# Kernel optimization log

Measured on AMD Instinct MI355X. Metric: run time of the kernel, lower is better.

## Reference

```python
import jax, jax.numpy as jnp
import numpy as np

B, S, HID = 2, 2048, 2048
NK, NV, DK, DV, K = 16, 32, 128, 128, 4
KEY_DIM = NK * DK          # 2048
VAL_DIM = NV * DV          # 4096
CONV_DIM = 2 * KEY_DIM + VAL_DIM  # 8192
EPS = 1e-6


def setup_inputs() -> dict:
    key = jax.random.key(0)
    ks = jax.random.split(key, 8)
    n = lambda k, shape, sc: jax.random.normal(k, shape, jnp.float32) * sc
    return {
        "hidden_states": n(ks[0], (B, S, HID), 1.0),
        "W_qkv": n(ks[1], (CONV_DIM, HID), 0.02),
        "W_z": n(ks[2], (VAL_DIM, HID), 0.02),
        "W_b": n(ks[3], (NV, HID), 0.02),
        "W_a": n(ks[4], (NV, HID), 0.02),
        "conv_w": n(ks[5], (CONV_DIM, K), 0.3),   # depthwise conv weight, squeeze(1) of [C,1,K]
        "norm_w": jnp.ones((DV,), jnp.float32),
        "W_out": n(ks[6], (HID, VAL_DIM), 0.02),
        "dt_bias": jnp.ones((NV,), jnp.float32),
        "A_log": jnp.zeros((NV,), jnp.float32),
    }


def _l2norm(t):
    return t * jax.lax.rsqrt(jnp.sum(t * t, axis=-1, keepdims=True) + EPS)


def _forward(hidden_states, W_qkv, W_z, W_b, W_a, conv_w, norm_w, W_out, dt_bias, A_log):
    b_, s_, _ = hidden_states.shape
    mixed = hidden_states @ W_qkv.T                     # [B,S,CONV_DIM]
    z = (hidden_states @ W_z.T).reshape(b_, s_, NV, DV)  # gate branch
    b_proj = hidden_states @ W_b.T                      # [B,S,NV]
    a_proj = hidden_states @ W_a.T                      # [B,S,NV]

    # causal depthwise conv1d (groups=CONV_DIM, no bias) + silu
    x = jnp.transpose(mixed, (0, 2, 1))                 # [B,C,S]
    x = jnp.pad(x, ((0, 0), (0, 0), (K - 1, 0)))
    x = jax.lax.conv_general_dilated(
        x, conv_w[:, None, :], window_strides=(1,), padding="VALID",
        feature_group_count=CONV_DIM)
    mixed = jnp.transpose(jax.nn.silu(x), (0, 2, 1))    # [B,S,CONV_DIM]

    q, k, v = jnp.split(mixed, [KEY_DIM, 2 * KEY_DIM], axis=-1)
    q = q.reshape(b_, s_, NK, DK)
    k = k.reshape(b_, s_, NK, DK)
    v = v.reshape(b_, s_, NV, DV)

    beta = jax.nn.sigmoid(b_proj)                                    # [B,S,NV]
    g = -jnp.exp(A_log) * jax.nn.softplus(a_proj + dt_bias)          # [B,S,NV], log decay

    rep = NV // NK
    q = jnp.repeat(q, rep, axis=2)                      # GQA expand -> [B,S,NV,DK]
    k = jnp.repeat(k, rep, axis=2)
    q = _l2norm(q)
    k = _l2norm(k)
    scale = DK ** -0.5

    def step(state, inp):  # state: [B,NV,DK,DV]
        qt, kt, vt, gt, bt = inp  # [B,NV,DK],[B,NV,DK],[B,NV,DV],[B,NV],[B,NV]
        state = state * jnp.exp(gt)[..., None, None]
        mem = jnp.einsum('bhk,bhkv->bhv', kt, state)
        delta = (vt - mem) * bt[..., None]
        state = state + jnp.einsum('bhk,bhv->bhkv', kt, delta)
        ot = jnp.einsum('bhk,bhkv->bhv', qt * scale, state)
        return state, ot

    init = jnp.zeros((b_, NV, DK, DV), jnp.float32)
    xs = (jnp.moveaxis(q, 1, 0), jnp.moveaxis(k, 1, 0), jnp.moveaxis(v, 1, 0),
          jnp.moveaxis(g, 1, 0), jnp.moveaxis(beta, 1, 0))
    _, o = jax.lax.scan(step, init, xs)                 # [S,B,NV,DV]
    o = jnp.moveaxis(o, 0, 1)                           # [B,S,NV,DV]

    # RMSNormGated over head_v_dim, then silu(z) gate
    var = jnp.mean(o * o, axis=-1, keepdims=True)
    o = o * jax.lax.rsqrt(var + EPS) * norm_w
    o = (o * jax.nn.silu(z)).reshape(b_, s_, VAL_DIM)
    return o @ W_out.T


def reference(hidden_states, W_qkv, W_z, W_b, W_a, conv_w, norm_w, W_out, dt_bias, A_log):
    return _forward(hidden_states, W_qkv, W_z, W_b, W_a, conv_w, norm_w, W_out, dt_bias, A_log)
```

## Files before the change

### kernel.cpp

```cpp
#include <hip/hip_runtime.h>
#include <hip/hip_bf16.h>
#include <math.h>

#define DEVI __device__ __forceinline__

typedef __attribute__((ext_vector_type(4))) float f32x4;
typedef __attribute__((ext_vector_type(8))) short s16x8;
typedef __attribute__((ext_vector_type(4))) unsigned int u32x4;

DEVI float bf2f(ushort u){ union{unsigned int i; float f;} x; x.i = ((unsigned int)u)<<16; return x.f; }
DEVI ushort f2bf(float f){ union{float f; unsigned int i;} x; x.f = f;
  unsigned int r = x.i + 0x7fffu + ((x.i>>16)&1u); return (ushort)(r>>16); }

#define MFMA16(a,b,c) __builtin_amdgcn_mfma_f32_16x16x32_bf16(a,b,c,0,0,0)

__global__ __launch_bounds__(256) void cvt_bf16(const float* __restrict__ in, ushort* __restrict__ out){
  int i = blockIdx.x*256 + threadIdx.x;
  float4 v = ((const float4*)in)[i];
  ushort4 o; o.x = f2bf(v.x); o.y = f2bf(v.y); o.z = f2bf(v.z); o.w = f2bf(v.w);
  ((ushort4*)out)[i] = o;
}

DEVI void gl_lds16(const ushort* g, ushort* l){
  __builtin_amdgcn_global_load_lds((const __attribute__((address_space(1))) void*)g,
                                   (__attribute__((address_space(3))) void*)l, 16, 0, 0);
}

#define SBAR() __builtin_amdgcn_s_barrier()
#define LGKM0() do{ asm volatile("s_waitcnt lgkmcnt(0)" ::: "memory"); __builtin_amdgcn_sched_barrier(0); }while(0)
#define VMC6() asm volatile("s_waitcnt vmcnt(6)" ::: "memory")
#define VMC4() asm volatile("s_waitcnt vmcnt(4)" ::: "memory")

template<int BF16_OUT>
__global__ __launch_bounds__(512, 2) void gemm256(const ushort* __restrict__ A,
                                                  const ushort* __restrict__ B,
                                                  void* __restrict__ Cv,
                                                  int M, int N, int K,
                                                  int rpx, int cpx){
  __shared__ ushort smem[65536];
  __shared__ ushort dummy[4096];
  const int tid = threadIdx.x, w = tid>>6, lane = tid&63;
  const int fr = lane&15, quad = lane>>4;
  const int wm = w>>2, wn = w&3;
  const int NT = K>>6;

  const int nbn = N>>8;
  const int bid = blockIdx.x;
  const int xcd = bid & 7, idx = bid >> 3;
  const int CGn = nbn / cpx;
  const int rgrp = xcd / CGn, cgrp = xcd % CGn;
  const int rloc = idx % rpx, cloc = idx / rpx;
  const long tileM = (long)(rgrp*rpx + rloc) << 8;
  const long tileN = (long)(cgrp*cpx + cloc) << 8;

  const int rr  = (tid&63)>>2;
  const int cc  = ((tid&3)*8) ^ ((rr&8)?16:0);
  const int row0 = (w>>1)*16 + rr;
  const int col0 = (w&1)*32 + cc;
  const long off0 = (long)row0*K + col0;
  const long h64 = 64l*K;

  const ushort* pA0 = A + tileM*K + off0;
  const ushort* pA1 = pA0 + 128l*K;
  const ushort* pB0 = B + tileN*K + off0;
  const ushort* pB1 = pB0 + 128l*K;

  const int dw = w*512;
  ushort* dmy = dummy + dw;

#define ST_A0(bb,tt) do{ if((tt)<NT){ const long kk=(long)(tt)<<6; \
    gl_lds16(pA0+kk, smem+(bb)*32768+dw);        gl_lds16(pA1+kk, smem+(bb)*32768+8192+dw);} \
    else { gl_lds16(pA0, dmy); gl_lds16(pA1, dmy);} }while(0)
#define ST_A1(bb,tt) do{ if((tt)<NT){ const long kk=((long)(tt)<<6)+h64; \
    gl_lds16(pA0+kk, smem+(bb)*32768+4096+dw);   gl_lds16(pA1+kk, smem+(bb)*32768+12288+dw);} \
    else { gl_lds16(pA0, dmy); gl_lds16(pA1, dmy);} }while(0)
#define ST_B0(bb,tt) do{ if((tt)<NT){ const long kk=(long)(tt)<<6; \
    gl_lds16(pB0+kk, smem+(bb)*32768+16384+dw);  gl_lds16(pB1+kk, smem+(bb)*32768+24576+dw);} \
    else { gl_lds16(pB0, dmy); gl_lds16(pB1, dmy);} }while(0)
#define ST_B1(bb,tt) do{ if((tt)<NT){ const long kk=((long)(tt)<<6)+h64; \
    gl_lds16(pB0+kk, smem+(bb)*32768+20480+dw);  gl_lds16(pB1+kk, smem+(bb)*32768+28672+dw);} \
    else { gl_lds16(pB0, dmy); gl_lds16(pB1, dmy);} }while(0)

  const int baseF = fr*32 + ((quad*8) ^ ((fr&8)?16:0));
  const int sB = (wn&1)*4;

  f32x4 acc[8][4];
  #pragma unroll
  for (int i=0;i<8;i++)
    #pragma unroll
    for (int j=0;j<4;j++) acc[i][j] = (f32x4){0.f,0.f,0.f,0.f};

  ST_A0(0,0); ST_B0(0,0); ST_B1(0,0); ST_A1(0,0);
  ST_A0(1,1); ST_B0(1,1); ST_B1(1,1);
  VMC6();
  SBAR();

  #pragma unroll 2
  for (int t=0; t<NT; ++t){
    const int bs = t&1;
    const ushort* SA = smem + bs*32768 + wm*8192;
    const ushort* SB = smem + bs*32768 + 16384 + (wn>>1)*8192;
    s16x8 af[4][2], bl[2][2], bh[2][2];
    #pragma unroll
    for (int mt=0;mt<4;mt++)
      #pragma unroll
      for (int ks=0;ks<2;ks++)
        af[mt][ks] = *(const s16x8*)(SA + ((mt*2+ks)<<9) + baseF);
    #pragma unroll
    for (int nt=0;nt<2;nt++)
      #pragma unroll
      for (int ks=0;ks<2;ks++)
        bl[nt][ks] = *(const s16x8*)(SB + (((sB+nt)*2+ks)<<9) + baseF);
    ST_A1(bs^1, t+1);
    SBAR(); LGKM0();
    __builtin_amdgcn_s_setprio(1);
    #pragma unroll
    for (int mt=0;mt<4;mt++)
      #pragma unroll
      for (int nt=0;nt<2;nt++){
        acc[mt][nt] = MFMA16(af[mt][0], bl[nt][0], acc[mt][nt]);
        acc[mt][nt] = MFMA16(af[mt][1], bl[nt][1], acc[mt][nt]);
      }
    __builtin_amdgcn_s_setprio(0);
    SBAR();
    #pragma unroll
    for (int nt=0;nt<2;nt++)
      #pragma unroll
      for (int ks=0;ks<2;ks++)
        bh[nt][ks] = *(const s16x8*)(SB + (((sB+2+nt)*2+ks)<<9) + baseF);
    ST_A0(bs, t+2);
    SBAR(); LGKM0();
    __builtin_amdgcn_s_setprio(1);
    #pragma unroll
    for (int mt=0;mt<4;mt++)
      #pragma unroll
      for (int nt=0;nt<2;nt++){
        acc[mt][2+nt] = MFMA16(af[mt][0], bh[nt][0], acc[mt][2+nt]);
        acc[mt][2+nt] = MFMA16(af[mt][1], bh[nt][1], acc[mt][2+nt]);
      }
    __builtin_amdgcn_s_setprio(0);
    SBAR();
    #pragma unroll
    for (int mt=0;mt<4;mt++)
      #pragma unroll
      for (int ks=0;ks<2;ks++)
        af[mt][ks] = *(const s16x8*)(SA + (((4+mt)*2+ks)<<9) + baseF);
    ST_B0(bs, t+2);
    SBAR(); LGKM0();
    __builtin_amdgcn_s_setprio(1);
    #pragma unroll
    for (int mt=0;mt<4;mt++)
      #pragma unroll
      for (int nt=0;nt<2;nt++){
        acc[4+mt][nt] = MFMA16(af[mt][0], bl[nt][0], acc[4+mt][nt]);
        acc[4+mt][nt] = MFMA16(af[mt][1], bl[nt][1], acc[4+mt][nt]);
      }
    __builtin_amdgcn_s_setprio(0);
    SBAR();
    ST_B1(bs, t+2);
    SBAR();
    __builtin_amdgcn_s_setprio(1);
    #pragma unroll
    for (int mt=0;mt<4;mt++)
      #pragma unroll
      for (int nt=0;nt<2;nt++){
        acc[4+mt][2+nt] = MFMA16(af[mt][0], bh[nt][0], acc[4+mt][2+nt]);
        acc[4+mt][2+nt] = MFMA16(af[mt][1], bh[nt][1], acc[4+mt][2+nt]);
      }
    __builtin_amdgcn_s_setprio(0);
    VMC6();
    SBAR();
  }
#undef ST_A0
#undef ST_A1
#undef ST_B0
#undef ST_B1

  const long Rb = tileM + wm*128 + quad*4;
  const long Cb = tileN + wn*64 + fr;
  if (BF16_OUT){
    ushort* C = (ushort*)Cv;
    #pragma unroll
    for (int mt=0;mt<8;mt++)
      #pragma unroll
      for (int r=0;r<4;r++){
        const long row = Rb + mt*16 + r;
        #pragma unroll
        for (int nt=0;nt<4;nt++)
          C[row*(long)N + Cb + nt*16] = f2bf(acc[mt][nt][r]);
      }
  } else {
    float* C = (float*)Cv;
    #pragma unroll
    for (int mt=0;mt<8;mt++)
      #pragma unroll
      for (int r=0;r<4;r++){
        const long row = Rb + mt*16 + r;
        #pragma unroll
        for (int nt=0;nt<4;nt++)
          C[row*(long)N + Cb + nt*16] = acc[mt][nt][r];
      }
  }
}

template<int BF16_OUT>
__global__ __launch_bounds__(512, 2) void gemm256n128(const ushort* __restrict__ A,
                                                      const ushort* __restrict__ B,
                                                      void* __restrict__ Cv,
                                                      int M, int N, int K,
                                                      int rpx, int cpx){
  __shared__ ushort smem[49152];
  __shared__ ushort dummy[4096];
  const int tid = threadIdx.x, w = tid>>6, lane = tid&63;
  const int fr = lane&15, quad = lane>>4;
  const int wm = w>>2, wn = w&3;
  const int NT = K>>6;

  const int nbn = N>>7;
  const int bid = blockIdx.x;
  const int xcd = bid & 7, idx = bid >> 3;
  const int CGn = nbn / cpx;
  const int rgrp = xcd / CGn, cgrp = xcd % CGn;
  const int rloc = idx % rpx, cloc = idx / rpx;
  const long tileM = (long)(rgrp*rpx + rloc) << 8;
  const long tileN = (long)(cgrp*cpx + cloc) << 7;

  const int rr  = (tid&63)>>2;
  const int cc  = ((tid&3)*8) ^ ((rr&8)?16:0);
  const int row0 = (w>>1)*16 + rr;
  const int col0 = (w&1)*32 + cc;
  const long off0 = (long)row0*K + col0;
  const long h64 = 64l*K;

  const ushort* pA0 = A + tileM*K + off0;
  const ushort* pA1 = pA0 + 128l*K;
  const ushort* pB0 = B + tileN*K + off0;

  const int dw = w*512;
  ushort* dmy = dummy + dw;

#define ST_A0(bb,tt) do{ if((tt)<NT){ const long kk=(long)(tt)<<6; \
    gl_lds16(pA0+kk, smem+(bb)*24576+dw);        gl_lds16(pA1+kk, smem+(bb)*24576+8192+dw);} \
    else { gl_lds16(pA0, dmy); gl_lds16(pA1, dmy);} }while(0)
#define ST_A1(bb,tt) do{ if((tt)<NT){ const long kk=((long)(tt)<<6)+h64; \
    gl_lds16(pA0+kk, smem+(bb)*24576+4096+dw);   gl_lds16(pA1+kk, smem+(bb)*24576+12288+dw);} \
    else { gl_lds16(pA0, dmy); gl_lds16(pA1, dmy);} }while(0)
#define ST_B(bb,tt) do{ if((tt)<NT){ const long kk=(long)(tt)<<6; \
    gl_lds16(pB0+kk, smem+(bb)*24576+16384+dw);  gl_lds16(pB0+kk+h64, smem+(bb)*24576+20480+dw);} \
    else { gl_lds16(pB0, dmy); gl_lds16(pB0, dmy);} }while(0)

  const int baseF = fr*32 + ((quad*8) ^ ((fr&8)?16:0));

  f32x4 acc[8][2];
  #pragma unroll
  for (int i=0;i<8;i++)
    #pragma unroll
    for (int j=0;j<2;j++) acc[i][j] = (f32x4){0.f,0.f,0.f,0.f};

  ST_A0(0,0); ST_B(0,0); ST_A1(0,0);
  ST_A0(1,1); ST_B(1,1);
  VMC4();
  SBAR();

  #pragma unroll 2
  for (int t=0; t<NT; ++t){
    const int bs = t&1;
    const ushort* SA = smem + bs*24576 + wm*8192;
    const ushort* SB = smem + bs*24576 + 16384;
    s16x8 af[4][2], bl[2], bh[2];
    #pragma unroll
    for (int mt=0;mt<4;mt++)
      #pragma unroll
      for (int ks=0;ks<2;ks++)
        af[mt][ks] = *(const s16x8*)(SA + ((mt*2+ks)<<9) + baseF);
    #pragma unroll
    for (int ks=0;ks<2;ks++)
      bl[ks] = *(const s16x8*)(SB + (((wn*2+0)*2+ks)<<9) + baseF);
    ST_A1(bs^1, t+1);
    SBAR(); LGKM0();
    __builtin_amdgcn_s_setprio(1);
    #pragma unroll
    for (int mt=0;mt<4;mt++){
      acc[mt][0] = MFMA16(af[mt][0], bl[0], acc[mt][0]);
      acc[mt][0] = MFMA16(af[mt][1], bl[1], acc[mt][0]);
    }
    __builtin_amdgcn_s_setprio(0);
    SBAR();
    #pragma unroll
    for (int ks=0;ks<2;ks++)
      bh[ks] = *(const s16x8*)(SB + (((wn*2+1)*2+ks)<<9) + baseF);
    ST_A0(bs, t+2);
    SBAR(); LGKM0();
    __builtin_amdgcn_s_setprio(1);
    #pragma unroll
    for (int mt=0;mt<4;mt++){
      acc[mt][1] = MFMA16(af[mt][0], bh[0], acc[mt][1]);
      acc[mt][1] = MFMA16(af[mt][1], bh[1], acc[mt][1]);
    }
    __builtin_amdgcn_s_setprio(0);
    SBAR();
    #pragma unroll
    for (int mt=0;mt<4;mt++)
      #pragma unroll
      for (int ks=0;ks<2;ks++)
        af[mt][ks] = *(const s16x8*)(SA + (((4+mt)*2+ks)<<9) + baseF);
    ST_B(bs, t+2);
    SBAR(); LGKM0();
    __builtin_amdgcn_s_setprio(1);
    #pragma unroll
    for (int mt=0;mt<4;mt++){
      acc[4+mt][0] = MFMA16(af[mt][0], bl[0], acc[4+mt][0]);
      acc[4+mt][0] = MFMA16(af[mt][1], bl[1], acc[4+mt][0]);
    }
    __builtin_amdgcn_s_setprio(0);
    SBAR();
    __builtin_amdgcn_s_setprio(1);
    #pragma unroll
    for (int mt=0;mt<4;mt++){
      acc[4+mt][1] = MFMA16(af[mt][0], bh[0], acc[4+mt][1]);
      acc[4+mt][1] = MFMA16(af[mt][1], bh[1], acc[4+mt][1]);
    }
    __builtin_amdgcn_s_setprio(0);
    VMC4();
    SBAR();
  }
#undef ST_A0
#undef ST_A1
#undef ST_B

  const long Rb = tileM + wm*128 + quad*4;
  const long Cb = tileN + wn*32 + fr;
  if (BF16_OUT){
    ushort* C = (ushort*)Cv;
    #pragma unroll
    for (int mt=0;mt<8;mt++)
      #pragma unroll
      for (int r=0;r<4;r++){
        const long row = Rb + mt*16 + r;
        #pragma unroll
        for (int nt=0;nt<2;nt++)
          C[row*(long)N + Cb + nt*16] = f2bf(acc[mt][nt][r]);
      }
  } else {
    float* C = (float*)Cv;
    #pragma unroll
    for (int mt=0;mt<8;mt++)
      #pragma unroll
      for (int r=0;r<4;r++){
        const long row = Rb + mt*16 + r;
        #pragma unroll
        for (int nt=0;nt<2;nt++)
          C[row*(long)N + Cb + nt*16] = acc[mt][nt][r];
      }
  }
}

template<int BF16_OUT>
__global__ __launch_bounds__(256, 2) void gemm_bt(const ushort* __restrict__ A,
                                                  const ushort* __restrict__ B,
                                                  void* __restrict__ Cv,
                                                  int M, int N, int K){
  __shared__ ushort As[128*32];
  __shared__ ushort Bs[128*32];
  const int nb = N >> 7;
  const int tile_m = (blockIdx.x / nb) << 7;
  const int tile_n = (blockIdx.x % nb) << 7;
  const int tid  = threadIdx.x;
  const int w    = tid >> 6;
  const int lane = tid & 63;

  const int ca = w*2;
  const long rowA = tile_m + ca*16 + (lane>>2);
  const long rowB = tile_n + ca*16 + (lane>>2);
  const int  colE = (lane&3)*8;
  const ushort* pA0 = A + rowA*(long)K + colE;
  const ushort* pA1 = pA0 + 16l*K;
  const ushort* pB0 = B + rowB*(long)K + colE;
  const ushort* pB1 = pB0 + 16l*K;
  ushort* lA0 = As + ca*512;
  ushort* lA1 = As + ca*512 + 512;
  ushort* lB0 = Bs + ca*512;
  ushort* lB1 = Bs + ca*512 + 512;

  const int wr = (w>>1)<<6;
  const int wc = (w&1)<<6;
  const int fr = lane & 15;
  const int fk = (lane>>4)<<3;

  f32x4 acc[4][4];
  #pragma unroll
  for (int i=0;i<4;i++)
    #pragma unroll
    for (int j=0;j<4;j++) acc[i][j] = (f32x4){0.f,0.f,0.f,0.f};

  for (int k0 = 0; k0 < K; k0 += 32){
    __syncthreads();
    gl_lds16(pA0, lA0);
    gl_lds16(pA1, lA1);
    gl_lds16(pB0, lB0);
    gl_lds16(pB1, lB1);
    __syncthreads();
    s16x8 af[4], bfr[4];
    #pragma unroll
    for (int t=0;t<4;t++){
      af[t]  = *(const s16x8*)(As + (wr + t*16 + fr)*32 + fk);
      bfr[t] = *(const s16x8*)(Bs + (wc + t*16 + fr)*32 + fk);
    }
    #pragma unroll
    for (int mt=0;mt<4;mt++)
      #pragma unroll
      for (int nt=0;nt<4;nt++)
        acc[mt][nt] = MFMA16(af[mt], bfr[nt], acc[mt][nt]);
    pA0 += 32; pA1 += 32; pB0 += 32; pB1 += 32;
  }

  const int crow = tile_m + wr + ((lane>>4)<<2);
  const int ccol = tile_n + wc + (lane&15);
  if (BF16_OUT){
    ushort* C = (ushort*)Cv;
    #pragma unroll
    for (int mt=0;mt<4;mt++)
      #pragma unroll
      for (int r=0;r<4;r++){
        long row = crow + mt*16 + r;
        #pragma unroll
        for (int nt=0;nt<4;nt++)
          C[row*(long)N + ccol + nt*16] = f2bf(acc[mt][nt][r]);
      }
  } else {
    float* C = (float*)Cv;
    #pragma unroll
    for (int mt=0;mt<4;mt++)
      #pragma unroll
      for (int r=0;r<4;r++){
        long row = crow + mt*16 + r;
        #pragma unroll
        for (int nt=0;nt<4;nt++)
          C[row*(long)N + ccol + nt*16] = acc[mt][nt][r];
      }
  }
}

__global__ __launch_bounds__(256) void ba_post(const float* __restrict__ bapr,
    const float* __restrict__ dtb, const float* __restrict__ alog,
    float* __restrict__ beta, float* __restrict__ glog){
  const int idx = blockIdx.x*256 + threadIdx.x;
  const int m = idx >> 6, j = idx & 63;
  const float v = bapr[(long)m*128 + j];
  if (j < 32){
    beta[(long)m*32 + j] = 1.f/(1.f+expf(-v));
  } else {
    const int n = j - 32;
    float ap = v + dtb[n];
    float sp = (ap > 20.f) ? ap : log1pf(expf(ap));
    glog[(long)m*32 + n] = -expf(alog[n]) * sp;
  }
}

__global__ __launch_bounds__(256) void conv_qkv2(const ushort* __restrict__ mixed,
    const float* __restrict__ convw, ushort* __restrict__ qn, ushort* __restrict__ kn,
    ushort* __restrict__ vv){
  const long m0 = (long)blockIdx.x * 32;
  const int ct = blockIdx.y;
  const int ch = (ct<<11) + threadIdx.x*8;
  const ushort* base = mixed + ch;

  ushort* outp; int mode; float qsc = 1.f;
  if (ct == 0){ outp = qn + ch;        mode = 0; qsc = 0.08838834764831845f; }
  else if (ct == 1){ outp = kn + (ch-2048); mode = 1; }
  else { outp = vv + (ch-4096); mode = 2; }

  float cw0[8], cw1[8], cw2[8], cw3[8];
  #pragma unroll
  for (int e=0;e<8;e++){
    float4 wv = *(const float4*)(convw + (long)(ch+e)*4);
    cw0[e]=wv.x; cw1[e]=wv.y; cw2[e]=wv.z; cw3[e]=wv.w;
  }

#define LDROW(PTR, R) do{ s16x8 _v = *(const s16x8*)(PTR); \
    _Pragma("unroll") \
    for (int e=0;e<8;e++) R[e] = bf2f((ushort)_v[e]); }while(0)

#define STEP(P0,P1,P2,P3,MR) do{ \
    float y[8]; float ss = 0.f; \
    _Pragma("unroll") \
    for (int e=0;e<8;e++){ \
      float a = P0[e]*cw0[e]; \
      a += P1[e]*cw1[e]; \
      a += P2[e]*cw2[e]; \
      a += P3[e]*cw3[e]; \
      float sv = a / (1.f + expf(-a)); \
      y[e] = sv; ss += sv*sv; } \
    if (mode < 2){ \
      ss += __shfl_xor(ss,1); ss += __shfl_xor(ss,2); \
      ss += __shfl_xor(ss,4); ss += __shfl_xor(ss,8); \
      const float r_ = rsqrtf(ss + 1e-6f) * qsc; \
      s16x8 ov; \
      _Pragma("unroll") \
      for (int e=0;e<8;e++) ov[e] = (short)f2bf(y[e]*r_); \
      *(s16x8*)(outp + (MR)*2048) = ov; \
    } else { \
      s16x8 ov; \
      _Pragma("unroll") \
      for (int e=0;e<8;e++) ov[e] = (short)f2bf(y[e]); \
      *(s16x8*)(outp + (MR)*4096) = ov; \
    } \
  }while(0)

  float w3[8], w2[8], w1[8];
  if (((int)m0 & 2047) == 0){
    #pragma unroll
    for (int e=0;e<8;e++){ w3[e]=0.f; w2[e]=0.f; w1[e]=0.f; }
  } else {
    LDROW(base + (m0-3)*8192, w3);
    LDROW(base + (m0-2)*8192, w2);
    LDROW(base + (m0-1)*8192, w1);
  }

  long m = m0;
  for (int it=0; it<8; ++it){
    float r0[8], r1[8], r2[8], r3[8];
    LDROW(base + (m+0)*8192, r0);
    LDROW(base + (m+1)*8192, r1);
    LDROW(base + (m+2)*8192, r2);
    LDROW(base + (m+3)*8192, r3);
    STEP(w3,w2,w1,r0, m+0);
    STEP(w2,w1,r0,r1, m+1);
    STEP(w1,r0,r1,r2, m+2);
    STEP(r0,r1,r2,r3, m+3);
    #pragma unroll
    for (int e=0;e<8;e++){ w3[e]=r1[e]; w2[e]=r2[e]; w1[e]=r3[e]; }
    m += 4;
  }
#undef LDROW
#undef STEP
}

__global__ __launch_bounds__(256) void chunk_prep(
    const ushort* __restrict__ qn, const ushort* __restrict__ kn,
    const float* __restrict__ beta, const float* __restrict__ glog,
    ushort* __restrict__ Tg, ushort* __restrict__ Mg, float* __restrict__ cumLgG){
  const int bid = blockIdx.x;
  const int bh = bid >> 6, ch = bid & 63;
  const int b = bh>>5, h = bh&31, hq = h>>1;
  const long tch = (long)b*2048 + ch*32;
  const int tid = threadIdx.x, w = tid>>6, lane = tid&63;
  const int quad = lane>>4, l15 = lane&15;

  __shared__ __attribute__((aligned(16))) ushort Kl[32][136];
  __shared__ __attribute__((aligned(16))) ushort Ql[32][136];
  __shared__ float Asl[32][33];
  __shared__ float Lgl[32], Btl[32];

  const int sc = tid>>3, ss = (tid&7)*16;
  {
    const ushort* kp = kn + (tch+sc)*2048 + hq*128 + ss;
    const ushort* qp = qn + (tch+sc)*2048 + hq*128 + ss;
    *(u32x4*)&Kl[sc][ss] = *(const u32x4*)kp; *(u32x4*)&Kl[sc][ss+8] = *(const u32x4*)(kp+8);
    *(u32x4*)&Ql[sc][ss] = *(const u32x4*)qp; *(u32x4*)&Ql[sc][ss+8] = *(const u32x4*)(qp+8);
  }
  if (tid < 64){
    const int c = lane & 31;
    float gv = glog[(tch + c)*32 + h];
    float bv = beta[(tch + c)*32 + h];
    #pragma unroll
    for (int off=1; off<32; off<<=1){
      float t = __shfl_up(gv, off);
      if ((lane & 31) >= off) gv += t;
    }
    if (lane < 32){ Lgl[c] = gv; Btl[c] = bv; cumLgG[(long)bid*32 + c] = gv; }
  }
  __syncthreads();

  const int mt = w>>1, nt = w&1;
  s16x8 ka[4], qa[4], kb[4];
  #pragma unroll
  for (int ks=0; ks<4; ks++){
    ka[ks] = *(const s16x8*)&Kl[mt*16+l15][ks*32 + quad*8];
    qa[ks] = *(const s16x8*)&Ql[mt*16+l15][ks*32 + quad*8];
    kb[ks] = *(const s16x8*)&Kl[nt*16+l15][ks*32 + quad*8];
  }
  f32x4 accK = (f32x4){0.f,0.f,0.f,0.f}, accQ = (f32x4){0.f,0.f,0.f,0.f};
  #pragma unroll
  for (int ks=0; ks<4; ks++){
    accK = MFMA16(ka[ks], kb[ks], accK);
    accQ = MFMA16(qa[ks], kb[ks], accQ);
  }
  const int j = nt*16 + l15;
  const float Lgj = Lgl[j];
  #pragma unroll
  for (int i=0;i<4;i++){
    const int r = mt*16 + quad*4 + i;
    const float e = expf(Lgl[r]-Lgj);
    Asl[r][j] = (r>j) ? -Btl[r]*e*accK[i] : 0.f;
    Mg[(long)bid*1024 + r*32 + j] = (r>=j) ? f2bf(e*accQ[i]) : (ushort)0;
  }
  __syncthreads();

  if (tid < 32){
    const int jc = tid;
    float tc[32];
    #pragma unroll
    for (int c=0;c<32;c++){
      float acc = (c==jc) ? 1.f : 0.f;
      #pragma unroll
      for (int i2=0;i2<c;i2++) acc = fmaf(Asl[c][i2], tc[i2], acc);
      tc[c] = acc;
      Tg[(long)bid*1024 + c*32 + jc] = f2bf(acc);
    }
  }
}

__global__ __launch_bounds__(256, 2) void chunk_scan3(
    const ushort* __restrict__ qn, const ushort* __restrict__ kn,
    const ushort* __restrict__ vv, const float* __restrict__ beta,
    const float* __restrict__ cumLg, const ushort* __restrict__ Tg,
    const ushort* __restrict__ Mg, float* __restrict__ o){
  const int bh = blockIdx.x & 63, sl = blockIdx.x >> 6;
  const int b = bh>>5, h = bh&31, hq = h>>1;
  const int dv0 = sl<<4;
  const int tid = threadIdx.x, w = tid>>6, lane = tid&63;
  const int quad = lane>>4, l15 = lane&15;
  const int rt = w&1, kq = w>>1;

  __shared__ __attribute__((aligned(16))) ushort STl[16][136];
  __shared__ __attribute__((aligned(16))) ushort B0T[16][40];
  __shared__ __attribute__((aligned(16))) ushort DT[16][40];
  __shared__ float Btf[32], eLgl[32], eDf[32];

  const ushort* pKQ = (kq ? qn : kn) + ((long)b*2048 + rt*16 + l15)*2048 + hq*128 + quad*8;
  const ushort* pKT = kn + ((long)b*2048 + quad*8)*2048 + hq*128 + w*32 + l15;
  const ushort* pV  = vv + ((long)b*2048 + rt*16 + quad*4)*4096 + h*128 + dv0 + l15;
  const ushort* pTM = (kq ? Mg : Tg) + (long)bh*65536 + (rt*16 + l15)*32 + quad*8;
  const long pbBase = (long)bh*2048 + tid;
  const float* betaP = beta + ((long)b*2048 + tid)*32 + h;

  s16x8 cKQ[4], nKQ[4], cK0, cK1, nK0, nK1, cTM, nTM;
  ushort cV0=0,cV1=0,cV2=0,cV3=0, nV0=0,nV1=0,nV2=0,nV3=0;
  float cLg = 0.f, nLg = 0.f, cBt = 0.f, nBt = 0.f;

  f32x4 S0 = (f32x4){0.f,0.f,0.f,0.f}, S1 = (f32x4){0.f,0.f,0.f,0.f};

#define LOADCH(PKQ,PK0,PK1,PV0,PV1,PV2,PV3,PTMv,PLG,PBT,CH) do{ \
    const long co = (long)(CH)*65536; \
    _Pragma("unroll") \
    for (int ks=0; ks<4; ks++) PKQ[ks] = *(const s16x8*)(pKQ + co + ks*32); \
    _Pragma("unroll") \
    for (int e=0; e<8; e++){ \
      PK0[e] = (short)pKT[co + (long)e*2048]; \
      PK1[e] = (short)pKT[co + (long)e*2048 + 16]; } \
    if (kq == 0){ \
      const long vo = (long)(CH)*131072; \
      PV0 = pV[vo]; PV1 = pV[vo+4096]; PV2 = pV[vo+8192]; PV3 = pV[vo+12288]; } \
    PTMv = *(const s16x8*)(pTM + (long)(CH)*1024); \
    if (tid < 32){ PLG = cumLg[pbBase + (long)(CH)*32]; PBT = betaP[(long)(CH)*1024]; } \
  }while(0)

  LOADCH(cKQ, cK0, cK1, cV0,cV1,cV2,cV3, cTM, cLg, cBt, 0);

  for (int ch=0; ch<64; ch++){
    const long tch = (long)b*2048 + ch*32;
    LOADCH(nKQ, nK0, nK1, nV0,nV1,nV2,nV3, nTM, nLg, nBt, (ch<63)?(ch+1):63);
    if (tid < 32){
      float lgC = __shfl(cLg, 31);
      Btf[tid] = cBt;
      eLgl[tid] = expf(cLg);
      eDf[tid]  = expf(lgC - cLg);
    }
    {
      ushort4 p0, p1;
      p0.x=f2bf(S0[0]); p0.y=f2bf(S0[1]); p0.z=f2bf(S0[2]); p0.w=f2bf(S0[3]);
      p1.x=f2bf(S1[0]); p1.y=f2bf(S1[1]); p1.z=f2bf(S1[2]); p1.w=f2bf(S1[3]);
      *(ushort4*)&STl[l15][w*32 + quad*4]      = p0;
      *(ushort4*)&STl[l15][w*32 + 16 + quad*4] = p1;
    }
    __syncthreads();
    f32x4 acc = (f32x4){0.f,0.f,0.f,0.f};
    #pragma unroll
    for (int ks=0; ks<4; ks++){
      s16x8 sb = *(const s16x8*)&STl[l15][ks*32 + quad*8];
      acc = MFMA16(cKQ[ks], sb, acc);
    }
    if (kq == 0){
      const int c0r = rt*16 + quad*4;
      ushort4 pb;
      pb.x = f2bf(Btf[c0r+0]*(bf2f(cV0) - eLgl[c0r+0]*acc[0]));
      pb.y = f2bf(Btf[c0r+1]*(bf2f(cV1) - eLgl[c0r+1]*acc[1]));
      pb.z = f2bf(Btf[c0r+2]*(bf2f(cV2) - eLgl[c0r+2]*acc[2]));
      pb.w = f2bf(Btf[c0r+3]*(bf2f(cV3) - eLgl[c0r+3]*acc[3]));
      *(ushort4*)&B0T[l15][rt*16 + quad*4] = pb;
    } else {
      #pragma unroll
      for (int i=0;i<4;i++) acc[i] *= eLgl[rt*16 + quad*4 + i];
    }
    __syncthreads();
    const float eC = eLgl[31];
    s16x8 kta0, kta1;
    #pragma unroll
    for (int e=0;e<8;e++){
      const float ed = eDf[quad*8 + e];
      kta0[e] = (short)f2bf(bf2f((ushort)cK0[e])*ed);
      kta1[e] = (short)f2bf(bf2f((ushort)cK1[e])*ed);
    }
    if (kq == 0){
      s16x8 a = *(const s16x8*)&B0T[l15][quad*8];
      f32x4 Dt = MFMA16(a, cTM, ((f32x4){0.f,0.f,0.f,0.f}));
      #pragma unroll
      for (int i=0;i<4;i++)
        DT[quad*4+i][rt*16 + l15] = f2bf(Dt[i]);
    }
    __syncthreads();
    s16x8 df = *(const s16x8*)&DT[l15][quad*8];
    if (kq == 1){
      f32x4 O = MFMA16(cTM, df, acc);
      #pragma unroll
      for (int i=0;i<4;i++)
        o[(tch + rt*16 + quad*4 + i)*4096 + h*128 + dv0 + l15] = O[i];
    }
    f32x4 t0, t1;
    #pragma unroll
    for (int i=0;i<4;i++){ t0[i] = S0[i]*eC; t1[i] = S1[i]*eC; }
    S0 = MFMA16(kta0, df, t0);
    S1 = MFMA16(kta1, df, t1);
    #pragma unroll
    for (int ks=0; ks<4; ks++) cKQ[ks] = nKQ[ks];
    cK0 = nK0; cK1 = nK1; cTM = nTM;
    cV0 = nV0; cV1 = nV1; cV2 = nV2; cV3 = nV3;
    cLg = nLg; cBt = nBt;
  }
#undef LOADCH
}

__global__ __launch_bounds__(128) void norm_gate(const float* __restrict__ o,
    const ushort* __restrict__ z, const float* __restrict__ normw,
    ushort* __restrict__ og){
  const long mh = blockIdx.x;
  const int d = threadIdx.x;
  float x = o[mh*128 + d];
  float ss = x*x;
  #pragma unroll
  for (int off=32; off; off>>=1) ss += __shfl_xor(ss, off);
  __shared__ float w2[2];
  if ((d&63)==0) w2[d>>6] = ss;
  __syncthreads();
  float r = rsqrtf((w2[0]+w2[1])*(1.f/128.f) + 1e-6f);
  float zz = bf2f(z[mh*128 + d]);
  float sil = zz / (1.f + expf(-zz));
  og[mh*128 + d] = f2bf(x*r*normw[d]*sil);
}

extern "C" void kernel_launch(void* const* d_in, const int* in_sizes, int n_in,
                              void* d_out, int out_size, void* d_ws, size_t ws_size,
                              hipStream_t stream){
  const float* hs    = (const float*)d_in[0];
  const float* Wqkv  = (const float*)d_in[1];
  const float* Wz    = (const float*)d_in[2];
  const float* Wb    = (const float*)d_in[3];
  const float* Wa    = (const float*)d_in[4];
  const float* convw = (const float*)d_in[5];
  const float* normw = (const float*)d_in[6];
  const float* Wout  = (const float*)d_in[7];
  const float* dtb   = (const float*)d_in[8];
  const float* alog  = (const float*)d_in[9];

  char* ws = (char*)d_ws;
  ushort* hsb   = (ushort*)(ws);
  ushort* wqb   = (ushort*)(ws + (16l<<20));
  ushort* wzb   = (ushort*)(ws + (48l<<20));
  ushort* wob   = (ushort*)(ws + (64l<<20));
  ushort* mixed = (ushort*)(ws + (80l<<20));
  ushort* zb    = (ushort*)(ws + (144l<<20));
  float*  beta  = (float*)(ws + (176l<<20));
  float*  cumLg = (float*)(ws + (176l<<20) + (512l<<10));
  float*  glog  = (float*)(ws + (177l<<20));
  ushort* Tg    = (ushort*)(ws + (178l<<20));
  ushort* Mg    = (ushort*)(ws + (186l<<20));
  ushort* wbab  = (ushort*)(ws + (194l<<20));
  float*  bapr  = (float*)(ws + (195l<<20));
  ushort* kn = hsb;  ushort* qn = wzb;  ushort* vvp = wqb;  ushort* og = wqb;
  float*  o_raw = (float*)mixed;

  cvt_bf16<<<8192,  256, 0, stream>>>(hs,   hsb);
  cvt_bf16<<<16384, 256, 0, stream>>>(Wqkv, wqb);
  cvt_bf16<<<8192,  256, 0, stream>>>(Wz,   wzb);
  cvt_bf16<<<8192,  256, 0, stream>>>(Wout, wob);
  cvt_bf16<<<64,    256, 0, stream>>>(Wb,   wbab);
  cvt_bf16<<<64,    256, 0, stream>>>(Wa,   wbab + 65536);

  gemm256<1><<<512, 512, 0, stream>>>(hsb, wqb, (void*)mixed, 4096, 8192, 2048, 4, 16);
  gemm256<1><<<256, 512, 0, stream>>>(hsb, wzb, (void*)zb,    4096, 4096, 2048, 4, 8);
  gemm_bt<0><<<32*1,  256, 0, stream>>>(hsb, wbab, (void*)bapr, 4096, 128,  2048);
  ba_post<<<1024, 256, 0, stream>>>(bapr, dtb, alog, beta, glog);

  conv_qkv2<<<dim3(128,4), 256, 0, stream>>>(mixed, convw, qn, kn, vvp);
  chunk_prep<<<4096, 256, 0, stream>>>(qn, kn, beta, glog, Tg, Mg, cumLg);
  chunk_scan3<<<512, 256, 0, stream>>>(qn, kn, vvp, beta, cumLg, Tg, Mg, o_raw);
  norm_gate<<<131072, 128, 0, stream>>>(o_raw, zb, normw, og);

  gemm256n128<0><<<256, 512, 0, stream>>>(og, wob, d_out, 4096, 2048, 4096, 4, 8);
}
```

Before: 697.8 us.

## Restructure GEMM mainloop to triple-buffered BK=32 stages with simpler schedule

Replaces the double-buffered BK=64 GEMM mainloop, which interleaved partial LDS loads with four MFMA sub-phases, with a triple-buffered BK=32 pipeline. Each iteration issues one stage load two steps ahead, waits on vmcnt, reads all A/B fragments and runs all 32 MFMAs. LDS use shrinks and the LDS swizzle changes to a new XOR pattern. The aim is deeper prefetch with fewer barriers per MFMA, at the cost of half the K work per barrier pair and less overlap of LDS reads with MFMA.

```diff
diff --git a/kernel.cpp b/kernel.cpp
--- a/kernel.cpp
+++ b/kernel.cpp
@@ -28,7 +28,7 @@
 
 #define SBAR() __builtin_amdgcn_s_barrier()
 #define LGKM0() do{ asm volatile("s_waitcnt lgkmcnt(0)" ::: "memory"); __builtin_amdgcn_sched_barrier(0); }while(0)
-#define VMC6() asm volatile("s_waitcnt vmcnt(6)" ::: "memory")
+#define VMC8() asm volatile("s_waitcnt vmcnt(8)" ::: "memory")
 #define VMC4() asm volatile("s_waitcnt vmcnt(4)" ::: "memory")
 
 template<int BF16_OUT>
@@ -37,12 +37,12 @@
                                                   void* __restrict__ Cv,
                                                   int M, int N, int K,
                                                   int rpx, int cpx){
-  __shared__ ushort smem[65536];
+  __shared__ ushort smem[49152];
   __shared__ ushort dummy[4096];
   const int tid = threadIdx.x, w = tid>>6, lane = tid&63;
   const int fr = lane&15, quad = lane>>4;
   const int wm = w>>2, wn = w&3;
-  const int NT = K>>6;
+  const int NT2 = K>>5;
 
   const int nbn = N>>8;
   const int bid = blockIdx.x;
@@ -53,36 +53,24 @@
   const long tileM = (long)(rgrp*rpx + rloc) << 8;
   const long tileN = (long)(cgrp*cpx + cloc) << 8;
 
-  const int rr  = (tid&63)>>2;
-  const int cc  = ((tid&3)*8) ^ ((rr&8)?16:0);
-  const int row0 = (w>>1)*16 + rr;
-  const int col0 = (w&1)*32 + cc;
-  const long off0 = (long)row0*K + col0;
-  const long h64 = 64l*K;
-
-  const ushort* pA0 = A + tileM*K + off0;
-  const ushort* pA1 = pA0 + 128l*K;
-  const ushort* pB0 = B + tileN*K + off0;
-  const ushort* pB1 = pB0 + 128l*K;
-
-  const int dw = w*512;
-  ushort* dmy = dummy + dw;
-
-#define ST_A0(bb,tt) do{ if((tt)<NT){ const long kk=(long)(tt)<<6; \
-    gl_lds16(pA0+kk, smem+(bb)*32768+dw);        gl_lds16(pA1+kk, smem+(bb)*32768+8192+dw);} \
-    else { gl_lds16(pA0, dmy); gl_lds16(pA1, dmy);} }while(0)
-#define ST_A1(bb,tt) do{ if((tt)<NT){ const long kk=((long)(tt)<<6)+h64; \
-    gl_lds16(pA0+kk, smem+(bb)*32768+4096+dw);   gl_lds16(pA1+kk, smem+(bb)*32768+12288+dw);} \
-    else { gl_lds16(pA0, dmy); gl_lds16(pA1, dmy);} }while(0)
-#define ST_B0(bb,tt) do{ if((tt)<NT){ const long kk=(long)(tt)<<6; \
-    gl_lds16(pB0+kk, smem+(bb)*32768+16384+dw);  gl_lds16(pB1+kk, smem+(bb)*32768+24576+dw);} \
-    else { gl_lds16(pB0, dmy); gl_lds16(pB1, dmy);} }while(0)
-#define ST_B1(bb,tt) do{ if((tt)<NT){ const long kk=((long)(tt)<<6)+h64; \
-    gl_lds16(pB0+kk, smem+(bb)*32768+20480+dw);  gl_lds16(pB1+kk, smem+(bb)*32768+28672+dw);} \
-    else { gl_lds16(pB0, dmy); gl_lds16(pB1, dmy);} }while(0)
-
-  const int baseF = fr*32 + ((quad*8) ^ ((fr&8)?16:0));
-  const int sB = (wn&1)*4;
+  const int srow = lane>>2;
+  const int scol = ((lane&3) ^ ((lane>>3)&3))*8;
+  const ushort* pSA = A + (tileM + w*16 + srow)*(long)K + scol;
+  const ushort* pSB = B + (tileN + w*16 + srow)*(long)K + scol;
+  const long h128 = 128l*K;
+  const int dwv = w*512;
+  ushort* dmy = dummy + dwv;
+
+#define STG(bb,tt) do{ if((tt)<NT2){ const long kk=(long)(tt)<<5; \
+    gl_lds16(pSA+kk,      smem+(bb)*16384+dwv); \
+    gl_lds16(pSA+kk+h128, smem+(bb)*16384+4096+dwv); \
+    gl_lds16(pSB+kk,      smem+(bb)*16384+8192+dwv); \
+    gl_lds16(pSB+kk+h128, smem+(bb)*16384+12288+dwv); } \
+    else { gl_lds16(pSA,dmy); gl_lds16(pSA,dmy); gl_lds16(pSB,dmy); gl_lds16(pSB,dmy);} }while(0)
+
+  const int swz = (quad ^ ((fr>>1)&3))*8;
+  const int laneA = (wm*128 + fr)*32 + swz;
+  const int laneB = 8192 + (wn*64 + fr)*32 + swz;
 
   f32x4 acc[8][4];
   #pragma unroll
@@ -90,91 +78,30 @@
     #pragma unroll
     for (int j=0;j<4;j++) acc[i][j] = (f32x4){0.f,0.f,0.f,0.f};
 
-  ST_A0(0,0); ST_B0(0,0); ST_B1(0,0); ST_A1(0,0);
-  ST_A0(1,1); ST_B0(1,1); ST_B1(1,1);
-  VMC6();
-  SBAR();
-
-  #pragma unroll 2
-  for (int t=0; t<NT; ++t){
-    const int bs = t&1;
-    const ushort* SA = smem + bs*32768 + wm*8192;
-    const ushort* SB = smem + bs*32768 + 16384 + (wn>>1)*8192;
-    s16x8 af[4][2], bl[2][2], bh[2][2];
-    #pragma unroll
-    for (int mt=0;mt<4;mt++)
-      #pragma unroll
-      for (int ks=0;ks<2;ks++)
-        af[mt][ks] = *(const s16x8*)(SA + ((mt*2+ks)<<9) + baseF);
-    #pragma unroll
-    for (int nt=0;nt<2;nt++)
-      #pragma unroll
-      for (int ks=0;ks<2;ks++)
-        bl[nt][ks] = *(const s16x8*)(SB + (((sB+nt)*2+ks)<<9) + baseF);
-    ST_A1(bs^1, t+1);
-    SBAR(); LGKM0();
+  STG(0,0); STG(1,1);
+
+  for (int t=0; t<NT2; ++t){
+    const int rb = t%3, sb = (t+2)%3;
+    STG(sb, t+2);
+    VMC8();
+    SBAR();
+    const ushort* BR = smem + rb*16384;
+    s16x8 af[8], bf[4];
+    #pragma unroll
+    for (int mt=0;mt<8;mt++) af[mt] = *(const s16x8*)(BR + laneA + mt*512);
+    #pragma unroll
+    for (int nt=0;nt<4;nt++) bf[nt] = *(const s16x8*)(BR + laneB + nt*512);
     __builtin_amdgcn_s_setprio(1);
     #pragma unroll
-    for (int mt=0;mt<4;mt++)
-      #pragma unroll
-      for (int nt=0;nt<2;nt++){
-        acc[mt][nt] = MFMA16(af[mt][0], bl[nt][0], acc[mt][nt]);
-        acc[mt][nt] = MFMA16(af[mt][1], bl[nt][1], acc[mt][nt]);
-      }
+    for (int mt=0;mt<8;mt++)
+      #pragma unroll
+      for (int nt=0;nt<4;nt++)
+        acc[mt][nt] = MFMA16(af[mt], bf[nt], acc[mt][nt]);
     __builtin_amdgcn_s_setprio(0);
+    LGKM0();
     SBAR();
-    #pragma unroll
-    for (int nt=0;nt<2;nt++)
-      #pragma unroll
-      for (int ks=0;ks<2;ks++)
-        bh[nt][ks] = *(const s16x8*)(SB + (((sB+2+nt)*2+ks)<<9) + baseF);
-    ST_A0(bs, t+2);
-    SBAR(); LGKM0();
-    __builtin_amdgcn_s_setprio(1);
-    #pragma unroll
-    for (int mt=0;mt<4;mt++)
-      #pragma unroll
-      for (int nt=0;nt<2;nt++){
-        acc[mt][2+nt] = MFMA16(af[mt][0], bh[nt][0], acc[mt][2+nt]);
-        acc[mt][2+nt] = MFMA16(af[mt][1], bh[nt][1], acc[mt][2+nt]);
-      }
-    __builtin_amdgcn_s_setprio(0);
-    SBAR();
-    #pragma unroll
-    for (int mt=0;mt<4;mt++)
-      #pragma unroll
-      for (int ks=0;ks<2;ks++)
-        af[mt][ks] = *(const s16x8*)(SA + (((4+mt)*2+ks)<<9) + baseF);
-    ST_B0(bs, t+2);
-    SBAR(); LGKM0();
-    __builtin_amdgcn_s_setprio(1);
-    #pragma unroll
-    for (int mt=0;mt<4;mt++)
-      #pragma unroll
-      for (int nt=0;nt<2;nt++){
-        acc[4+mt][nt] = MFMA16(af[mt][0], bl[nt][0], acc[4+mt][nt]);
-        acc[4+mt][nt] = MFMA16(af[mt][1], bl[nt][1], acc[4+mt][nt]);
-      }
-    __builtin_amdgcn_s_setprio(0);
-    SBAR();
-    ST_B1(bs, t+2);
-    SBAR();
-    __builtin_amdgcn_s_setprio(1);
-    #pragma unroll
-    for (int mt=0;mt<4;mt++)
-      #pragma unroll
-      for (int nt=0;nt<2;nt++){
-        acc[4+mt][2+nt] = MFMA16(af[mt][0], bh[nt][0], acc[4+mt][2+nt]);
-        acc[4+mt][2+nt] = MFMA16(af[mt][1], bh[nt][1], acc[4+mt][2+nt]);
-      }
-    __builtin_amdgcn_s_setprio(0);
-    VMC6();
-    SBAR();
-  }
-#undef ST_A0
-#undef ST_A1
-#undef ST_B0
-#undef ST_B1
+  }
+#undef STG
 
   const long Rb = tileM + wm*128 + quad*4;
   const long Cb = tileN + wn*64 + fr;
```

New measurement: 712.2 us. +2.1%, slower.
